# Performance work log

Measured on AMD Instinct MI355X. Metric: run time of the kernel, lower is better.

## Reference

```python
import jax, jax.numpy as jnp
import numpy as np

N = 100000
E = 1600000
F_IN = 512
H1, C1 = 8, 8          # conv1: 8 heads x 8 channels, concat -> 64
H2, C2 = 1, 16         # conv2: 1 head x num_classes=16, mean
NEG_SLOPE = 0.2


def setup_inputs() -> dict:
    key = jax.random.key(0)
    ks = jax.random.split(key, 10)
    x = jax.random.normal(ks[0], (N, F_IN), dtype=jnp.float32)
    edge_index = jax.random.randint(ks[1], (2, E), 0, N, dtype=jnp.int64)
    s1 = 1.0 / np.sqrt(F_IN)
    s2 = 1.0 / np.sqrt(H1 * C1)
    W1 = jax.random.normal(ks[2], (F_IN, H1 * C1), dtype=jnp.float32) * s1
    a1_src = jax.random.normal(ks[3], (H1, C1), dtype=jnp.float32) * 0.1
    a1_dst = jax.random.normal(ks[4], (H1, C1), dtype=jnp.float32) * 0.1
    b1 = jnp.zeros((H1 * C1,), dtype=jnp.float32)
    W2 = jax.random.normal(ks[5], (H1 * C1, H2 * C2), dtype=jnp.float32) * s2
    a2_src = jax.random.normal(ks[6], (H2, C2), dtype=jnp.float32) * 0.1
    a2_dst = jax.random.normal(ks[7], (H2, C2), dtype=jnp.float32) * 0.1
    b2 = jnp.zeros((C2,), dtype=jnp.float32)
    return {"x": x, "edge_index": edge_index, "W1": W1, "a1_src": a1_src,
            "a1_dst": a1_dst, "b1": b1, "W2": W2, "a2_src": a2_src,
            "a2_dst": a2_dst, "b2": b2}


def _add_self_loops(edge_index, n):
    loops = jnp.arange(n, dtype=edge_index.dtype)
    return jnp.concatenate([edge_index, jnp.stack([loops, loops])], axis=1)


def gat_conv(x, edge_index, W, a_src, a_dst, bias, concat):
    # x: [N, Fin]; W: [Fin, H*C]; a_*: [H, C]
    n = x.shape[0]
    H, C = a_src.shape
    h = (x @ W).reshape(n, H, C)                      # [N, H, C]
    al_src = jnp.einsum('nhc,hc->nh', h, a_src)       # [N, H]
    al_dst = jnp.einsum('nhc,hc->nh', h, a_dst)
    src, dst = edge_index[0], edge_index[1]
    e = al_src[src] + al_dst[dst]                     # [E, H]
    e = jnp.where(e > 0, e, NEG_SLOPE * e)            # LeakyReLU
    # segment softmax over destination nodes
    m = jax.ops.segment_max(e, dst, num_segments=n)   # [N, H]
    ex = jnp.exp(e - m[dst])
    s = jax.ops.segment_sum(ex, dst, num_segments=n)  # [N, H]
    alpha = ex / s[dst]                               # [E, H]
    msg = h[src] * alpha[:, :, None]                  # [E, H, C]
    out = jax.ops.segment_sum(msg, dst, num_segments=n)  # [N, H, C]
    if concat:
        out = out.reshape(n, H * C)
    else:
        out = out.mean(axis=1)
    return out + bias


def reference(x, edge_index, W1, a1_src, a1_dst, b1, W2, a2_src, a2_dst, b2):
    ei = _add_self_loops(edge_index, x.shape[0])
    h = gat_conv(x, ei, W1, a1_src, a1_dst, b1, concat=True)
    h = jax.nn.elu(h)
    h = gat_conv(h, ei, W2, a2_src, a2_dst, b2, concat=False)
    return jax.nn.log_softmax(h, axis=1)
```

## Files before the change

### kernel.cpp

```cpp
#include <hip/hip_runtime.h>
#include <math.h>

#define F_IN 512
#define NHEAD1 8
#define NC1 8
#define F1 64
#define NC2 16
#define NEG_SLOPE 0.2f
#define BSHIFT 7
#define PART_G 512
#define BUILD_CAP 4608

static __device__ __forceinline__ float leaky(float v) {
    return v > 0.0f ? v : NEG_SLOPE * v;
}

__global__ __launch_bounds__(256) void k_gemm1(const float* __restrict__ x,
                                               const float* __restrict__ W,
                                               const float* __restrict__ a1s,
                                               const float* __restrict__ a1d,
                                               float* __restrict__ h1,
                                               float* __restrict__ al1s,
                                               float* __restrict__ al1d, int N) {
    __shared__ float xs[32][68];
    __shared__ float wsm[32][64];
    const int tid = threadIdx.x;
    const int tx = tid & 15, ty = tid >> 4;
    const int row0 = blockIdx.x * 64;
    const int r = tid & 63;
    const int kq = tid >> 6;
    float acc[4][4] = {};

    for (int k0 = 0; k0 < F_IN; k0 += 32) {
        {
            int gr = row0 + r;
            float4 v0 = make_float4(0.f, 0.f, 0.f, 0.f), v1 = v0;
            if (gr < N) {
                const float* p = x + (size_t)gr * F_IN + k0 + kq * 8;
                v0 = *(const float4*)p;
                v1 = *(const float4*)(p + 4);
            }
            xs[kq * 8 + 0][r] = v0.x; xs[kq * 8 + 1][r] = v0.y;
            xs[kq * 8 + 2][r] = v0.z; xs[kq * 8 + 3][r] = v0.w;
            xs[kq * 8 + 4][r] = v1.x; xs[kq * 8 + 5][r] = v1.y;
            xs[kq * 8 + 6][r] = v1.z; xs[kq * 8 + 7][r] = v1.w;
            int wr = tid >> 4;
            int wc = (tid & 15) * 4;
            #pragma unroll
            for (int rr = 0; rr < 32; rr += 16) {
                *(float4*)(&wsm[wr + rr][wc]) =
                    *(const float4*)(W + (size_t)(k0 + wr + rr) * F1 + wc);
            }
        }
        __syncthreads();
        #pragma unroll
        for (int k = 0; k < 32; ++k) {
            float4 a = *(const float4*)(&xs[k][ty * 4]);
            float4 b = *(const float4*)(&wsm[k][tx * 4]);
            acc[0][0] = fmaf(a.x, b.x, acc[0][0]); acc[0][1] = fmaf(a.x, b.y, acc[0][1]);
            acc[0][2] = fmaf(a.x, b.z, acc[0][2]); acc[0][3] = fmaf(a.x, b.w, acc[0][3]);
            acc[1][0] = fmaf(a.y, b.x, acc[1][0]); acc[1][1] = fmaf(a.y, b.y, acc[1][1]);
            acc[1][2] = fmaf(a.y, b.z, acc[1][2]); acc[1][3] = fmaf(a.y, b.w, acc[1][3]);
            acc[2][0] = fmaf(a.z, b.x, acc[2][0]); acc[2][1] = fmaf(a.z, b.y, acc[2][1]);
            acc[2][2] = fmaf(a.z, b.z, acc[2][2]); acc[2][3] = fmaf(a.z, b.w, acc[2][3]);
            acc[3][0] = fmaf(a.w, b.x, acc[3][0]); acc[3][1] = fmaf(a.w, b.y, acc[3][1]);
            acc[3][2] = fmaf(a.w, b.z, acc[3][2]); acc[3][3] = fmaf(a.w, b.w, acc[3][3]);
        }
        __syncthreads();
    }
    const int h = tx >> 1;
    const float* as = a1s + h * 8 + (tx & 1) * 4;
    const float* ad = a1d + h * 8 + (tx & 1) * 4;
    float4 asv = *(const float4*)as;
    float4 adv = *(const float4*)ad;
    #pragma unroll
    for (int i = 0; i < 4; ++i) {
        int gr = row0 + ty * 4 + i;
        float ps = acc[i][0] * asv.x + acc[i][1] * asv.y
                 + acc[i][2] * asv.z + acc[i][3] * asv.w;
        float pd = acc[i][0] * adv.x + acc[i][1] * adv.y
                 + acc[i][2] * adv.z + acc[i][3] * adv.w;
        ps += __shfl_xor(ps, 1);
        pd += __shfl_xor(pd, 1);
        if (gr < N) {
            *(float4*)(h1 + (size_t)gr * F1 + tx * 4) =
                make_float4(acc[i][0], acc[i][1], acc[i][2], acc[i][3]);
            if ((tx & 1) == 0) {
                al1s[gr * 8 + h] = ps;
                al1d[gr * 8 + h] = pd;
            }
        }
    }
}

__global__ __launch_bounds__(256) void k_bcount(const int* __restrict__ ei,
                                                int* __restrict__ counts,
                                                int E, int NBUCK, int chunk) {
    __shared__ int cnt[1024];
    const int g = blockIdx.x, tid = threadIdx.x;
    for (int i = tid; i < NBUCK; i += 256) cnt[i] = 0;
    __syncthreads();
    int lo = g * chunk, hi = lo + chunk;
    if (hi > E) hi = E;
    for (int e = lo + tid; e < hi; e += 256)
        atomicAdd(&cnt[ei[E + e] >> BSHIFT], 1);
    __syncthreads();
    for (int k = tid; k < NBUCK; k += 256)
        counts[k * PART_G + g] = cnt[k];
}

__global__ __launch_bounds__(256) void k_scan_block(const int* __restrict__ in,
                                                    int* __restrict__ out,
                                                    int* __restrict__ blocksum, int L) {
    __shared__ int sdata[256];
    int t = threadIdx.x;
    int i = blockIdx.x * 256 + t;
    int v = (i < L) ? in[i] : 0;
    sdata[t] = v;
    __syncthreads();
    for (int off = 1; off < 256; off <<= 1) {
        int add = (t >= off) ? sdata[t - off] : 0;
        __syncthreads();
        sdata[t] += add;
        __syncthreads();
    }
    if (i < L) out[i] = sdata[t] - v;
    if (t == 255) blocksum[blockIdx.x] = sdata[t];
}

__global__ void k_scan_carry(const int* __restrict__ blocksum,
                             int* __restrict__ blockoffset, int NB) {
    int lane = threadIdx.x;
    int carry = 0;
    for (int base = 0; base < NB; base += 64) {
        int i = base + lane;
        int v = (i < NB) ? blocksum[i] : 0;
        int x = v;
        #pragma unroll
        for (int off = 1; off < 64; off <<= 1) {
            int y = __shfl_up(x, off);
            if (lane >= off) x += y;
        }
        if (i < NB) blockoffset[i] = carry + x - v;
        carry += __shfl(x, 63);
    }
}

__global__ __launch_bounds__(256) void k_bscatter(const int* __restrict__ ei,
                                                  const int* __restrict__ offs,
                                                  const int* __restrict__ boff,
                                                  unsigned* __restrict__ packed,
                                                  int E, int NBUCK, int chunk) {
    __shared__ int cur[1024];
    const int g = blockIdx.x, tid = threadIdx.x;
    for (int k = tid; k < NBUCK; k += 256) {
        int idx = k * PART_G + g;
        cur[k] = offs[idx] + boff[idx >> 8];
    }
    __syncthreads();
    int lo = g * chunk, hi = lo + chunk;
    if (hi > E) hi = E;
    for (int e = lo + tid; e < hi; e += 256) {
        int src = ei[e], dst = ei[E + e];
        int pos = atomicAdd(&cur[dst >> BSHIFT], 1);
        packed[pos] = ((unsigned)(dst & 127) << 20) | (unsigned)src;
    }
}

__global__ __launch_bounds__(256) void k_bbuild(const unsigned* __restrict__ packed,
                                                const int* __restrict__ offs,
                                                const int* __restrict__ boff,
                                                int* __restrict__ rowptr,
                                                int* __restrict__ esrc,
                                                int E, int N, int NBUCK) {
    __shared__ int sdeg[128], sinc[128], scur[128];
    __shared__ int sbuf[BUILD_CAP];
    const int k = blockIdx.x, tid = threadIdx.x;
    const int i0 = k * PART_G;
    const int s = offs[i0] + boff[i0 >> 8];
    int e;
    if (k + 1 < NBUCK) {
        int i1 = (k + 1) * PART_G;
        e = offs[i1] + boff[i1 >> 8];
    } else e = E;
    const int cnt = e - s;
    if (tid < 128) sdeg[tid] = 0;
    __syncthreads();
    for (int i = tid; i < cnt; i += 256)
        atomicAdd(&sdeg[packed[s + i] >> 20], 1);
    __syncthreads();
    if (tid < 128) sinc[tid] = sdeg[tid];
    __syncthreads();
    for (int off = 1; off < 128; off <<= 1) {
        int add = (tid < 128 && tid >= off) ? sinc[tid - off] : 0;
        __syncthreads();
        if (tid < 128) sinc[tid] += add;
        __syncthreads();
    }
    int nd = N - (k << BSHIFT);
    if (nd > 128) nd = 128;
    if (tid < nd) {
        int excl = sinc[tid] - sdeg[tid];
        rowptr[(k << BSHIFT) + tid] = s + excl;
        scur[tid] = excl;
    }
    if (k == 0 && tid == 0) rowptr[N] = E;
    __syncthreads();
    if (cnt <= BUILD_CAP) {
        for (int i = tid; i < cnt; i += 256) {
            unsigned p = packed[s + i];
            int pos = atomicAdd(&scur[p >> 20], 1);
            sbuf[pos] = (int)(p & 0xFFFFFu);
        }
        __syncthreads();
        for (int i = tid; i < cnt; i += 256) esrc[s + i] = sbuf[i];
    } else {
        for (int i = tid; i < cnt; i += 256) {
            unsigned p = packed[s + i];
            int pos = atomicAdd(&scur[p >> 20], 1);
            esrc[s + pos] = (int)(p & 0xFFFFFu);
        }
    }
}

__global__ __launch_bounds__(256) void k_agg1(
    const float* __restrict__ h1, const float* __restrict__ al1s,
    const float* __restrict__ al1d, const int* __restrict__ rowptr,
    const int* __restrict__ esrc, const float* __restrict__ b1,
    const float* __restrict__ W2, const float* __restrict__ a2s,
    const float* __restrict__ a2d, float* __restrict__ h2,
    float* __restrict__ al2s, float* __restrict__ al2d, int N) {
    const int lane = threadIdx.x & 63;
    const int wv = threadIdx.x >> 6;
    const int n = blockIdx.x * 4 + wv;
    if (n >= N) return;
    const int sub = lane >> 4;
    const int t = lane & 15;
    const int h = t >> 1;

    float4 w2r[4];
    #pragma unroll
    for (int j = 0; j < 4; ++j)
        w2r[j] = *(const float4*)(W2 + (4 * t + j) * NC2 + 4 * sub);
    const float4 b1v  = *(const float4*)(b1 + 4 * t);
    const float4 a2sv = *(const float4*)(a2s + 4 * sub);
    const float4 a2dv = *(const float4*)(a2d + 4 * sub);

    const float aldh = al1d[n * 8 + h];
    float s = 0.f, acc0 = 0.f, acc1 = 0.f, acc2 = 0.f, acc3 = 0.f;
    if (sub == 0) {
        float w0 = __expf(leaky(al1s[n * 8 + h] + aldh));
        float4 u = *(const float4*)(h1 + (size_t)n * F1 + t * 4);
        s = w0;
        acc0 = w0 * u.x; acc1 = w0 * u.y; acc2 = w0 * u.z; acc3 = w0 * u.w;
    }
    const int start = rowptr[n], end = rowptr[n + 1];
    for (int base = start; base < end; base += 64) {
        int cnt = end - base;
        if (cnt > 64) cnt = 64;
        int msrc = (lane < cnt) ? esrc[base + lane] : 0;
        for (int j4 = 0; j4 < cnt; j4 += 4) {
            int idx = j4 + sub;
            int src = __shfl(msrc, idx);
            float w = (idx < cnt) ? __expf(leaky(al1s[src * 8 + h] + aldh)) : 0.f;
            float4 u = *(const float4*)(h1 + (size_t)src * F1 + t * 4);
            s += w;
            acc0 = fmaf(w, u.x, acc0);
            acc1 = fmaf(w, u.y, acc1);
            acc2 = fmaf(w, u.z, acc2);
            acc3 = fmaf(w, u.w, acc3);
        }
    }
    #pragma unroll
    for (int off = 16; off < 64; off <<= 1) {
        s    += __shfl_xor(s, off);
        acc0 += __shfl_xor(acc0, off);
        acc1 += __shfl_xor(acc1, off);
        acc2 += __shfl_xor(acc2, off);
        acc3 += __shfl_xor(acc3, off);
    }
    float rs = 1.0f / s;
    float v0 = acc0 * rs + b1v.x; v0 = v0 > 0.f ? v0 : expm1f(v0);
    float v1 = acc1 * rs + b1v.y; v1 = v1 > 0.f ? v1 : expm1f(v1);
    float v2 = acc2 * rs + b1v.z; v2 = v2 > 0.f ? v2 : expm1f(v2);
    float v3 = acc3 * rs + b1v.w; v3 = v3 > 0.f ? v3 : expm1f(v3);
    float p0 = v0 * w2r[0].x + v1 * w2r[1].x + v2 * w2r[2].x + v3 * w2r[3].x;
    float p1 = v0 * w2r[0].y + v1 * w2r[1].y + v2 * w2r[2].y + v3 * w2r[3].y;
    float p2 = v0 * w2r[0].z + v1 * w2r[1].z + v2 * w2r[2].z + v3 * w2r[3].z;
    float p3 = v0 * w2r[0].w + v1 * w2r[1].w + v2 * w2r[2].w + v3 * w2r[3].w;
    #pragma unroll
    for (int off = 1; off < 16; off <<= 1) {
        p0 += __shfl_xor(p0, off);
        p1 += __shfl_xor(p1, off);
        p2 += __shfl_xor(p2, off);
        p3 += __shfl_xor(p3, off);
    }
    float ts = p0 * a2sv.x + p1 * a2sv.y + p2 * a2sv.z + p3 * a2sv.w;
    float td = p0 * a2dv.x + p1 * a2dv.y + p2 * a2dv.z + p3 * a2dv.w;
    ts += __shfl_xor(ts, 16); ts += __shfl_xor(ts, 32);
    td += __shfl_xor(td, 16); td += __shfl_xor(td, 32);
    if (t == 0)
        *(float4*)(h2 + (size_t)n * NC2 + sub * 4) = make_float4(p0, p1, p2, p3);
    if (lane == 0) { al2s[n] = ts; al2d[n] = td; }
}

__global__ __launch_bounds__(256) void k_agg2(
    const float* __restrict__ h2, const float* __restrict__ al2s,
    const float* __restrict__ al2d, const int* __restrict__ rowptr,
    const int* __restrict__ esrc, const float* __restrict__ b2,
    float* __restrict__ out, int N) {
    const int lane = threadIdx.x & 63;
    const int wv = threadIdx.x >> 6;
    const int n = blockIdx.x * 4 + wv;
    if (n >= N) return;
    const int sub = lane >> 3;
    const int t = lane & 7;
    const float ald = al2d[n];
    float s = 0.f, a0 = 0.f, a1 = 0.f;
    if (sub == 0) {
        float w0 = __expf(leaky(al2s[n] + ald));
        float2 u = *(const float2*)(h2 + (size_t)n * NC2 + t * 2);
        s = w0;
        a0 = w0 * u.x;
        a1 = w0 * u.y;
    }
    const int start = rowptr[n], end = rowptr[n + 1];
    for (int base = start; base < end; base += 64) {
        int cnt = end - base;
        if (cnt > 64) cnt = 64;
        int msrc = (lane < cnt) ? esrc[base + lane] : 0;
        for (int j8 = 0; j8 < cnt; j8 += 8) {
            int idx = j8 + sub;
            int src = __shfl(msrc, idx);
            float w = (idx < cnt) ? __expf(leaky(al2s[src] + ald)) : 0.f;
            float2 u = *(const float2*)(h2 + (size_t)src * NC2 + t * 2);
            s += w;
            a0 = fmaf(w, u.x, a0);
            a1 = fmaf(w, u.y, a1);
        }
    }
    #pragma unroll
    for (int off = 8; off < 64; off <<= 1) {
        s  += __shfl_xor(s, off);
        a0 += __shfl_xor(a0, off);
        a1 += __shfl_xor(a1, off);
    }
    float rs = 1.0f / s;
    float2 b2v = *(const float2*)(b2 + 2 * t);
    float v0 = a0 * rs + b2v.x;
    float v1 = a1 * rs + b2v.y;
    float mm = fmaxf(v0, v1);
    #pragma unroll
    for (int off = 1; off < 8; off <<= 1) mm = fmaxf(mm, __shfl_xor(mm, off));
    float se = __expf(v0 - mm) + __expf(v1 - mm);
    #pragma unroll
    for (int off = 1; off < 8; off <<= 1) se += __shfl_xor(se, off);
    float l = logf(se) + mm;
    if (sub == 0)
        *(float2*)(out + (size_t)n * NC2 + 2 * t) = make_float2(v0 - l, v1 - l);
}

extern "C" void kernel_launch(void* const* d_in, const int* in_sizes, int n_in,
                              void* d_out, int out_size, void* d_ws, size_t ws_size,
                              hipStream_t stream) {
    const float* x      = (const float*)d_in[0];
    const int*   ei     = (const int*)d_in[1];
    const float* W1     = (const float*)d_in[2];
    const float* a1_src = (const float*)d_in[3];
    const float* a1_dst = (const float*)d_in[4];
    const float* b1     = (const float*)d_in[5];
    const float* W2     = (const float*)d_in[6];
    const float* a2_src = (const float*)d_in[7];
    const float* a2_dst = (const float*)d_in[8];
    const float* b2     = (const float*)d_in[9];
    float* out = (float*)d_out;

    const int N = in_sizes[0] / F_IN;
    const int E = in_sizes[1] / 2;
    const int NH = N * NHEAD1;
    const int NBUCK = (N + 127) >> BSHIFT;
    const int L = NBUCK * PART_G;
    const int NB = (L + 255) / 256;
    const int chunk = (E + PART_G - 1) / PART_G;

    char* base = (char*)d_ws;
    size_t off = 0;
    auto alloc = [&](size_t bytes, size_t align) -> void* {
        off = (off + align - 1) & ~(align - 1);
        void* p = base + off; off += bytes; return p;
    };
    float* h1   = (float*)alloc((size_t)N * F1 * 4, 16);
    float* al1s = (float*)alloc((size_t)NH * 4, 16);
    float* al1d = (float*)alloc((size_t)NH * 4, 16);
    float* h2   = (float*)alloc((size_t)N * NC2 * 4, 16);
    float* al2s = (float*)alloc((size_t)N * 4, 16);
    float* al2d = (float*)alloc((size_t)N * 4, 16);
    int* rowptr = (int*)alloc((size_t)(N + 1) * 4, 16);
    int* esrc   = (int*)alloc((size_t)E * 4, 16);
    char* tbase = (char*)h1;
    unsigned* packed = (unsigned*)tbase;
    int* counts   = (int*)(tbase + (size_t)E * 4);
    int* offs     = counts + L;
    int* blocksum = offs + L;
    int* boffset  = blocksum + NB;

    const int B = 256;
    auto blocks = [](long long cnt, int b) { return (int)((cnt + b - 1) / b); };

    k_bcount<<<PART_G, 256, 0, stream>>>(ei, counts, E, NBUCK, chunk);
    k_scan_block<<<NB, 256, 0, stream>>>(counts, offs, blocksum, L);
    k_scan_carry<<<1, 64, 0, stream>>>(blocksum, boffset, NB);
    k_bscatter<<<PART_G, 256, 0, stream>>>(ei, offs, boffset, packed, E, NBUCK, chunk);
    k_bbuild<<<NBUCK, 256, 0, stream>>>(packed, offs, boffset, rowptr, esrc, E, N, NBUCK);

    k_gemm1<<<dim3((N + 63) / 64), dim3(256), 0, stream>>>(x, W1, a1_src, a1_dst,
                                                           h1, al1s, al1d, N);
    k_agg1<<<blocks(N, 4), 256, 0, stream>>>(h1, al1s, al1d, rowptr, esrc,
                                             b1, W2, a2_src, a2_dst,
                                             h2, al2s, al2d, N);
    k_agg2<<<blocks(N, 4), 256, 0, stream>>>(h2, al2s, al2d, rowptr, esrc, b2, out, N);
}
```

Baseline: 573.2 us.

## Store node features h1 and h2 in fp16 and remap aggregation lanes

The GEMM now writes the layer-1 node features as half precision, and layer 1 writes its transformed features the same way. Both aggregation kernels gather fp16 rows and accumulate in fp32. Lanes are remapped so each lane handles 8 (layer 1) or 4 (layer 2) channels, which lets more edges be processed per wave step. This halves the random-gather traffic and roughly doubles edge parallelism per wave. The cost is fp16 rounding error in the intermediate features and more registers per lane.

```diff
diff --git a/kernel.cpp b/kernel.cpp
--- a/kernel.cpp
+++ b/kernel.cpp
@@ -1,4 +1,5 @@
 #include <hip/hip_runtime.h>
+#include <hip/hip_fp16.h>
 #include <math.h>
 
 #define F_IN 512
@@ -19,7 +20,7 @@
                                                const float* __restrict__ W,
                                                const float* __restrict__ a1s,
                                                const float* __restrict__ a1d,
-                                               float* __restrict__ h1,
+                                               __half* __restrict__ h1h,
                                                float* __restrict__ al1s,
                                                float* __restrict__ al1d, int N) {
     __shared__ float xs[32][68];
@@ -83,8 +84,10 @@
         ps += __shfl_xor(ps, 1);
         pd += __shfl_xor(pd, 1);
         if (gr < N) {
-            *(float4*)(h1 + (size_t)gr * F1 + tx * 4) =
-                make_float4(acc[i][0], acc[i][1], acc[i][2], acc[i][3]);
+            union { __half2 h2v[2]; float2 f; } cv;
+            cv.h2v[0] = __floats2half2_rn(acc[i][0], acc[i][1]);
+            cv.h2v[1] = __floats2half2_rn(acc[i][2], acc[i][3]);
+            *(float2*)(h1h + (size_t)gr * F1 + tx * 4) = cv.f;
             if ((tx & 1) == 0) {
                 al1s[gr * 8 + h] = ps;
                 al1d[gr * 8 + h] = pd;
@@ -224,105 +227,33 @@
 }
 
 __global__ __launch_bounds__(256) void k_agg1(
-    const float* __restrict__ h1, const float* __restrict__ al1s,
+    const __half* __restrict__ h1h, const float* __restrict__ al1s,
     const float* __restrict__ al1d, const int* __restrict__ rowptr,
     const int* __restrict__ esrc, const float* __restrict__ b1,
     const float* __restrict__ W2, const float* __restrict__ a2s,
-    const float* __restrict__ a2d, float* __restrict__ h2,
+    const float* __restrict__ a2d, __half* __restrict__ h2h,
     float* __restrict__ al2s, float* __restrict__ al2d, int N) {
-    const int lane = threadIdx.x & 63;
-    const int wv = threadIdx.x >> 6;
-    const int n = blockIdx.x * 4 + wv;
-    if (n >= N) return;
-    const int sub = lane >> 4;
-    const int t = lane & 15;
-    const int h = t >> 1;
-
-    float4 w2r[4];
-    #pragma unroll
-    for (int j = 0; j < 4; ++j)
-        w2r[j] = *(const float4*)(W2 + (4 * t + j) * NC2 + 4 * sub);
-    const float4 b1v  = *(const float4*)(b1 + 4 * t);
-    const float4 a2sv = *(const float4*)(a2s + 4 * sub);
-    const float4 a2dv = *(const float4*)(a2d + 4 * sub);
-
-    const float aldh = al1d[n * 8 + h];
-    float s = 0.f, acc0 = 0.f, acc1 = 0.f, acc2 = 0.f, acc3 = 0.f;
-    if (sub == 0) {
-        float w0 = __expf(leaky(al1s[n * 8 + h] + aldh));
-        float4 u = *(const float4*)(h1 + (size_t)n * F1 + t * 4);
-        s = w0;
-        acc0 = w0 * u.x; acc1 = w0 * u.y; acc2 = w0 * u.z; acc3 = w0 * u.w;
-    }
-    const int start = rowptr[n], end = rowptr[n + 1];
-    for (int base = start; base < end; base += 64) {
-        int cnt = end - base;
-        if (cnt > 64) cnt = 64;
-        int msrc = (lane < cnt) ? esrc[base + lane] : 0;
-        for (int j4 = 0; j4 < cnt; j4 += 4) {
-            int idx = j4 + sub;
-            int src = __shfl(msrc, idx);
-            float w = (idx < cnt) ? __expf(leaky(al1s[src * 8 + h] + aldh)) : 0.f;
-            float4 u = *(const float4*)(h1 + (size_t)src * F1 + t * 4);
-            s += w;
-            acc0 = fmaf(w, u.x, acc0);
-            acc1 = fmaf(w, u.y, acc1);
-            acc2 = fmaf(w, u.z, acc2);
-            acc3 = fmaf(w, u.w, acc3);
-        }
-    }
-    #pragma unroll
-    for (int off = 16; off < 64; off <<= 1) {
-        s    += __shfl_xor(s, off);
-        acc0 += __shfl_xor(acc0, off);
-        acc1 += __shfl_xor(acc1, off);
-        acc2 += __shfl_xor(acc2, off);
-        acc3 += __shfl_xor(acc3, off);
-    }
-    float rs = 1.0f / s;
-    float v0 = acc0 * rs + b1v.x; v0 = v0 > 0.f ? v0 : expm1f(v0);
-    float v1 = acc1 * rs + b1v.y; v1 = v1 > 0.f ? v1 : expm1f(v1);
-    float v2 = acc2 * rs + b1v.z; v2 = v2 > 0.f ? v2 : expm1f(v2);
-    float v3 = acc3 * rs + b1v.w; v3 = v3 > 0.f ? v3 : expm1f(v3);
-    float p0 = v0 * w2r[0].x + v1 * w2r[1].x + v2 * w2r[2].x + v3 * w2r[3].x;
-    float p1 = v0 * w2r[0].y + v1 * w2r[1].y + v2 * w2r[2].y + v3 * w2r[3].y;
-    float p2 = v0 * w2r[0].z + v1 * w2r[1].z + v2 * w2r[2].z + v3 * w2r[3].z;
-    float p3 = v0 * w2r[0].w + v1 * w2r[1].w + v2 * w2r[2].w + v3 * w2r[3].w;
-    #pragma unroll
-    for (int off = 1; off < 16; off <<= 1) {
-        p0 += __shfl_xor(p0, off);
-        p1 += __shfl_xor(p1, off);
-        p2 += __shfl_xor(p2, off);
-        p3 += __shfl_xor(p3, off);
-    }
-    float ts = p0 * a2sv.x + p1 * a2sv.y + p2 * a2sv.z + p3 * a2sv.w;
-    float td = p0 * a2dv.x + p1 * a2dv.y + p2 * a2dv.z + p3 * a2dv.w;
-    ts += __shfl_xor(ts, 16); ts += __shfl_xor(ts, 32);
-    td += __shfl_xor(td, 16); td += __shfl_xor(td, 32);
-    if (t == 0)
-        *(float4*)(h2 + (size_t)n * NC2 + sub * 4) = make_float4(p0, p1, p2, p3);
-    if (lane == 0) { al2s[n] = ts; al2d[n] = td; }
-}
-
-__global__ __launch_bounds__(256) void k_agg2(
-    const float* __restrict__ h2, const float* __restrict__ al2s,
-    const float* __restrict__ al2d, const int* __restrict__ rowptr,
-    const int* __restrict__ esrc, const float* __restrict__ b2,
-    float* __restrict__ out, int N) {
     const int lane = threadIdx.x & 63;
     const int wv = threadIdx.x >> 6;
     const int n = blockIdx.x * 4 + wv;
     if (n >= N) return;
     const int sub = lane >> 3;
     const int t = lane & 7;
-    const float ald = al2d[n];
-    float s = 0.f, a0 = 0.f, a1 = 0.f;
+
+    const float aldh = al1d[n * 8 + t];
+    float s = 0.f;
+    float acc[8] = {};
     if (sub == 0) {
-        float w0 = __expf(leaky(al2s[n] + ald));
-        float2 u = *(const float2*)(h2 + (size_t)n * NC2 + t * 2);
+        float w0 = __expf(leaky(al1s[n * 8 + t] + aldh));
+        float4 raw = *(const float4*)(h1h + (size_t)n * F1 + t * 8);
+        const __half2* hp = (const __half2*)&raw;
         s = w0;
-        a0 = w0 * u.x;
-        a1 = w0 * u.y;
+        #pragma unroll
+        for (int q = 0; q < 4; ++q) {
+            float2 c = __half22float2(hp[q]);
+            acc[2 * q]     = w0 * c.x;
+            acc[2 * q + 1] = w0 * c.y;
+        }
     }
     const int start = rowptr[n], end = rowptr[n + 1];
     for (int base = start; base < end; base += 64) {
@@ -332,32 +263,127 @@
         for (int j8 = 0; j8 < cnt; j8 += 8) {
             int idx = j8 + sub;
             int src = __shfl(msrc, idx);
+            float w = (idx < cnt) ? __expf(leaky(al1s[src * 8 + t] + aldh)) : 0.f;
+            float4 raw = *(const float4*)(h1h + (size_t)src * F1 + t * 8);
+            const __half2* hp = (const __half2*)&raw;
+            s += w;
+            #pragma unroll
+            for (int q = 0; q < 4; ++q) {
+                float2 c = __half22float2(hp[q]);
+                acc[2 * q]     = fmaf(w, c.x, acc[2 * q]);
+                acc[2 * q + 1] = fmaf(w, c.y, acc[2 * q + 1]);
+            }
+        }
+    }
+    #pragma unroll
+    for (int off = 8; off < 64; off <<= 1) {
+        s += __shfl_xor(s, off);
+        #pragma unroll
+        for (int q = 0; q < 8; ++q) acc[q] += __shfl_xor(acc[q], off);
+    }
+    float rs = 1.0f / s;
+    const float4 b1a = *(const float4*)(b1 + 8 * t);
+    const float4 b1b = *(const float4*)(b1 + 8 * t + 4);
+    float v[8];
+    v[0] = acc[0] * rs + b1a.x; v[1] = acc[1] * rs + b1a.y;
+    v[2] = acc[2] * rs + b1a.z; v[3] = acc[3] * rs + b1a.w;
+    v[4] = acc[4] * rs + b1b.x; v[5] = acc[5] * rs + b1b.y;
+    v[6] = acc[6] * rs + b1b.z; v[7] = acc[7] * rs + b1b.w;
+    #pragma unroll
+    for (int q = 0; q < 8; ++q) v[q] = v[q] > 0.f ? v[q] : expm1f(v[q]);
+    float p0 = 0.f, p1 = 0.f;
+    #pragma unroll
+    for (int c = 0; c < 8; ++c) {
+        float2 wrow = *(const float2*)(W2 + (size_t)(8 * t + c) * NC2 + 2 * sub);
+        p0 = fmaf(v[c], wrow.x, p0);
+        p1 = fmaf(v[c], wrow.y, p1);
+    }
+    #pragma unroll
+    for (int off = 1; off < 8; off <<= 1) {
+        p0 += __shfl_xor(p0, off);
+        p1 += __shfl_xor(p1, off);
+    }
+    const float2 a2sv = *(const float2*)(a2s + 2 * sub);
+    const float2 a2dv = *(const float2*)(a2d + 2 * sub);
+    float ts = p0 * a2sv.x + p1 * a2sv.y;
+    float td = p0 * a2dv.x + p1 * a2dv.y;
+    #pragma unroll
+    for (int off = 8; off < 64; off <<= 1) {
+        ts += __shfl_xor(ts, off);
+        td += __shfl_xor(td, off);
+    }
+    if (t == 0)
+        *(__half2*)(h2h + (size_t)n * NC2 + 2 * sub) = __floats2half2_rn(p0, p1);
+    if (lane == 0) { al2s[n] = ts; al2d[n] = td; }
+}
+
+__global__ __launch_bounds__(256) void k_agg2(
+    const __half* __restrict__ h2h, const float* __restrict__ al2s,
+    const float* __restrict__ al2d, const int* __restrict__ rowptr,
+    const int* __restrict__ esrc, const float* __restrict__ b2,
+    float* __restrict__ out, int N) {
+    const int lane = threadIdx.x & 63;
+    const int wv = threadIdx.x >> 6;
+    const int n = blockIdx.x * 4 + wv;
+    if (n >= N) return;
+    const int sub = lane >> 2;
+    const int t = lane & 3;
+    const float ald = al2d[n];
+    float s = 0.f, a0 = 0.f, a1 = 0.f, a2 = 0.f, a3 = 0.f;
+    if (sub == 0) {
+        float w0 = __expf(leaky(al2s[n] + ald));
+        float2 raw = *(const float2*)(h2h + (size_t)n * NC2 + 4 * t);
+        const __half2* hp = (const __half2*)&raw;
+        float2 c01 = __half22float2(hp[0]);
+        float2 c23 = __half22float2(hp[1]);
+        s = w0;
+        a0 = w0 * c01.x; a1 = w0 * c01.y;
+        a2 = w0 * c23.x; a3 = w0 * c23.y;
+    }
+    const int start = rowptr[n], end = rowptr[n + 1];
+    for (int base = start; base < end; base += 64) {
+        int cnt = end - base;
+        if (cnt > 64) cnt = 64;
+        int msrc = (lane < cnt) ? esrc[base + lane] : 0;
+        for (int j16 = 0; j16 < cnt; j16 += 16) {
+            int idx = j16 + sub;
+            int src = __shfl(msrc, idx);
             float w = (idx < cnt) ? __expf(leaky(al2s[src] + ald)) : 0.f;
-            float2 u = *(const float2*)(h2 + (size_t)src * NC2 + t * 2);
+            float2 raw = *(const float2*)(h2h + (size_t)src * NC2 + 4 * t);
+            const __half2* hp = (const __half2*)&raw;
+            float2 c01 = __half22float2(hp[0]);
+            float2 c23 = __half22float2(hp[1]);
             s += w;
-            a0 = fmaf(w, u.x, a0);
-            a1 = fmaf(w, u.y, a1);
-        }
-    }
-    #pragma unroll
-    for (int off = 8; off < 64; off <<= 1) {
+            a0 = fmaf(w, c01.x, a0);
+            a1 = fmaf(w, c01.y, a1);
+            a2 = fmaf(w, c23.x, a2);
+            a3 = fmaf(w, c23.y, a3);
+        }
+    }
+    #pragma unroll
+    for (int off = 4; off < 64; off <<= 1) {
         s  += __shfl_xor(s, off);
         a0 += __shfl_xor(a0, off);
         a1 += __shfl_xor(a1, off);
+        a2 += __shfl_xor(a2, off);
+        a3 += __shfl_xor(a3, off);
     }
     float rs = 1.0f / s;
-    float2 b2v = *(const float2*)(b2 + 2 * t);
+    const float4 b2v = *(const float4*)(b2 + 4 * t);
     float v0 = a0 * rs + b2v.x;
     float v1 = a1 * rs + b2v.y;
-    float mm = fmaxf(v0, v1);
-    #pragma unroll
-    for (int off = 1; off < 8; off <<= 1) mm = fmaxf(mm, __shfl_xor(mm, off));
-    float se = __expf(v0 - mm) + __expf(v1 - mm);
-    #pragma unroll
-    for (int off = 1; off < 8; off <<= 1) se += __shfl_xor(se, off);
+    float v2 = a2 * rs + b2v.z;
+    float v3 = a3 * rs + b2v.w;
+    float mm = fmaxf(fmaxf(v0, v1), fmaxf(v2, v3));
+    #pragma unroll
+    for (int off = 1; off < 4; off <<= 1) mm = fmaxf(mm, __shfl_xor(mm, off));
+    float se = __expf(v0 - mm) + __expf(v1 - mm) + __expf(v2 - mm) + __expf(v3 - mm);
+    #pragma unroll
+    for (int off = 1; off < 4; off <<= 1) se += __shfl_xor(se, off);
     float l = logf(se) + mm;
     if (sub == 0)
-        *(float2*)(out + (size_t)n * NC2 + 2 * t) = make_float2(v0 - l, v1 - l);
+        *(float4*)(out + (size_t)n * NC2 + 4 * t) =
+            make_float4(v0 - l, v1 - l, v2 - l, v3 - l);
 }
 
 extern "C" void kernel_launch(void* const* d_in, const int* in_sizes, int n_in,
@@ -389,22 +415,21 @@
         off = (off + align - 1) & ~(align - 1);
         void* p = base + off; off += bytes; return p;
     };
-    float* h1   = (float*)alloc((size_t)N * F1 * 4, 16);
+    __half* h1h = (__half*)alloc((size_t)N * F1 * 2, 16);
     float* al1s = (float*)alloc((size_t)NH * 4, 16);
     float* al1d = (float*)alloc((size_t)NH * 4, 16);
-    float* h2   = (float*)alloc((size_t)N * NC2 * 4, 16);
+    __half* h2h = (__half*)alloc((size_t)N * NC2 * 2, 16);
     float* al2s = (float*)alloc((size_t)N * 4, 16);
     float* al2d = (float*)alloc((size_t)N * 4, 16);
     int* rowptr = (int*)alloc((size_t)(N + 1) * 4, 16);
     int* esrc   = (int*)alloc((size_t)E * 4, 16);
-    char* tbase = (char*)h1;
+    char* tbase = (char*)h1h;
     unsigned* packed = (unsigned*)tbase;
     int* counts   = (int*)(tbase + (size_t)E * 4);
     int* offs     = counts + L;
     int* blocksum = offs + L;
     int* boffset  = blocksum + NB;
 
-    const int B = 256;
     auto blocks = [](long long cnt, int b) { return (int)((cnt + b - 1) / b); };
 
     k_bcount<<<PART_G, 256, 0, stream>>>(ei, counts, E, NBUCK, chunk);
@@ -414,9 +439,9 @@
     k_bbuild<<<NBUCK, 256, 0, stream>>>(packed, offs, boffset, rowptr, esrc, E, N, NBUCK);
 
     k_gemm1<<<dim3((N + 63) / 64), dim3(256), 0, stream>>>(x, W1, a1_src, a1_dst,
-                                                           h1, al1s, al1d, N);
-    k_agg1<<<blocks(N, 4), 256, 0, stream>>>(h1, al1s, al1d, rowptr, esrc,
+                                                           h1h, al1s, al1d, N);
+    k_agg1<<<blocks(N, 4), 256, 0, stream>>>(h1h, al1s, al1d, rowptr, esrc,
                                              b1, W2, a2_src, a2_dst,
-                                             h2, al2s, al2d, N);
-    k_agg2<<<blocks(N, 4), 256, 0, stream>>>(h2, al2s, al2d, rowptr, esrc, b2, out, N);
-}
+                                             h2h, al2s, al2d, N);
+    k_agg2<<<blocks(N, 4), 256, 0, stream>>>(h2h, al2s, al2d, rowptr, esrc, b2, out, N);
+}
```

New measurement: 584.3 us. About the same (+1.9%).

## Use fp16 MFMA for first-layer GEMM and store layer-2 features in half

Applied to the files above, without the earlier changes.

Rewrites the x@W1 GEMM to convert inputs to fp16 and use the 16x16x32 f16 MFMA instruction, with a small prep kernel that transposes W1 to fp16. The second-layer features h2 are stored as half, and k_agg2 gives each lane 4 channels so 16 edges are processed per pass instead of 8. The intent is to replace slow scalar FP32 FMA with matrix cores and halve gather bandwidth in agg2, at the cost of fp16 rounding error.

```diff
diff --git a/kernel.cpp b/kernel.cpp
--- a/kernel.cpp
+++ b/kernel.cpp
@@ -1,4 +1,5 @@
 #include <hip/hip_runtime.h>
+#include <hip/hip_fp16.h>
 #include <math.h>
 
 #define F_IN 512
@@ -11,83 +12,97 @@
 #define PART_G 512
 #define BUILD_CAP 4608
 
+typedef _Float16 v8h __attribute__((ext_vector_type(8)));
+typedef float v4f __attribute__((ext_vector_type(4)));
+
 static __device__ __forceinline__ float leaky(float v) {
     return v > 0.0f ? v : NEG_SLOPE * v;
 }
 
+__global__ __launch_bounds__(256) void k_prep(const float* __restrict__ W,
+                                              _Float16* __restrict__ w1t) {
+    int idx = blockIdx.x * 256 + threadIdx.x;
+    if (idx < 64 * 512) {
+        int c = idx >> 9, k = idx & 511;
+        w1t[idx] = (_Float16)W[k * 64 + c];
+    }
+}
+
 __global__ __launch_bounds__(256) void k_gemm1(const float* __restrict__ x,
-                                               const float* __restrict__ W,
+                                               const _Float16* __restrict__ w1t,
                                                const float* __restrict__ a1s,
                                                const float* __restrict__ a1d,
                                                float* __restrict__ h1,
                                                float* __restrict__ al1s,
                                                float* __restrict__ al1d, int N) {
-    __shared__ float xs[32][68];
-    __shared__ float wsm[32][64];
+    __shared__ _Float16 xs[64][72];
+    __shared__ _Float16 ws[64][72];
     const int tid = threadIdx.x;
-    const int tx = tid & 15, ty = tid >> 4;
+    const int lane = tid & 63;
+    const int wv = tid >> 6;
     const int row0 = blockIdx.x * 64;
-    const int r = tid & 63;
-    const int kq = tid >> 6;
-    float acc[4][4] = {};
-
-    for (int k0 = 0; k0 < F_IN; k0 += 32) {
-        {
-            int gr = row0 + r;
-            float4 v0 = make_float4(0.f, 0.f, 0.f, 0.f), v1 = v0;
+    const int srow = tid >> 2;
+    const int skq = (tid & 3) * 16;
+    v4f acc[4] = {};
+
+    for (int k0 = 0; k0 < F_IN; k0 += 64) {
+        int gr = row0 + srow;
+        float4 v0, v1, v2, v3;
+        if (gr < N) {
+            const float* p = x + (size_t)gr * F_IN + k0 + skq;
+            v0 = *(const float4*)p;       v1 = *(const float4*)(p + 4);
+            v2 = *(const float4*)(p + 8); v3 = *(const float4*)(p + 12);
+        } else {
+            v0 = make_float4(0.f, 0.f, 0.f, 0.f); v1 = v0; v2 = v0; v3 = v0;
+        }
+        const _Float16* q = w1t + (size_t)srow * F_IN + k0 + skq;
+        v8h wa = *(const v8h*)q;
+        v8h wb = *(const v8h*)(q + 8);
+        v8h xa, xb;
+        xa[0] = (_Float16)v0.x; xa[1] = (_Float16)v0.y;
+        xa[2] = (_Float16)v0.z; xa[3] = (_Float16)v0.w;
+        xa[4] = (_Float16)v1.x; xa[5] = (_Float16)v1.y;
+        xa[6] = (_Float16)v1.z; xa[7] = (_Float16)v1.w;
+        xb[0] = (_Float16)v2.x; xb[1] = (_Float16)v2.y;
+        xb[2] = (_Float16)v2.z; xb[3] = (_Float16)v2.w;
+        xb[4] = (_Float16)v3.x; xb[5] = (_Float16)v3.y;
+        xb[6] = (_Float16)v3.z; xb[7] = (_Float16)v3.w;
+        __syncthreads();
+        *(v8h*)&xs[srow][skq]     = xa;
+        *(v8h*)&xs[srow][skq + 8] = xb;
+        *(v8h*)&ws[srow][skq]     = wa;
+        *(v8h*)&ws[srow][skq + 8] = wb;
+        __syncthreads();
+        #pragma unroll
+        for (int kk = 0; kk < 64; kk += 32) {
+            v8h a = *(const v8h*)&xs[wv * 16 + (lane & 15)][kk + (lane >> 4) * 8];
+            #pragma unroll
+            for (int c4 = 0; c4 < 4; ++c4) {
+                v8h b = *(const v8h*)&ws[c4 * 16 + (lane & 15)][kk + (lane >> 4) * 8];
+                acc[c4] = __builtin_amdgcn_mfma_f32_16x16x32_f16(a, b, acc[c4], 0, 0, 0);
+            }
+        }
+    }
+    const int g = lane >> 4;
+    const int cl = lane & 15;
+    #pragma unroll
+    for (int c4 = 0; c4 < 4; ++c4) {
+        float asv = a1s[c4 * 16 + cl];
+        float adv = a1d[c4 * 16 + cl];
+        #pragma unroll
+        for (int r = 0; r < 4; ++r) {
+            int gr = row0 + wv * 16 + g * 4 + r;
+            float vacc = acc[c4][r];
+            float ps = vacc * asv, pd = vacc * adv;
+            ps += __shfl_xor(ps, 1); ps += __shfl_xor(ps, 2); ps += __shfl_xor(ps, 4);
+            pd += __shfl_xor(pd, 1); pd += __shfl_xor(pd, 2); pd += __shfl_xor(pd, 4);
             if (gr < N) {
-                const float* p = x + (size_t)gr * F_IN + k0 + kq * 8;
-                v0 = *(const float4*)p;
-                v1 = *(const float4*)(p + 4);
-            }
-            xs[kq * 8 + 0][r] = v0.x; xs[kq * 8 + 1][r] = v0.y;
-            xs[kq * 8 + 2][r] = v0.z; xs[kq * 8 + 3][r] = v0.w;
-            xs[kq * 8 + 4][r] = v1.x; xs[kq * 8 + 5][r] = v1.y;
-            xs[kq * 8 + 6][r] = v1.z; xs[kq * 8 + 7][r] = v1.w;
-            int wr = tid >> 4;
-            int wc = (tid & 15) * 4;
-            #pragma unroll
-            for (int rr = 0; rr < 32; rr += 16) {
-                *(float4*)(&wsm[wr + rr][wc]) =
-                    *(const float4*)(W + (size_t)(k0 + wr + rr) * F1 + wc);
-            }
-        }
-        __syncthreads();
-        #pragma unroll
-        for (int k = 0; k < 32; ++k) {
-            float4 a = *(const float4*)(&xs[k][ty * 4]);
-            float4 b = *(const float4*)(&wsm[k][tx * 4]);
-            acc[0][0] = fmaf(a.x, b.x, acc[0][0]); acc[0][1] = fmaf(a.x, b.y, acc[0][1]);
-            acc[0][2] = fmaf(a.x, b.z, acc[0][2]); acc[0][3] = fmaf(a.x, b.w, acc[0][3]);
-            acc[1][0] = fmaf(a.y, b.x, acc[1][0]); acc[1][1] = fmaf(a.y, b.y, acc[1][1]);
-            acc[1][2] = fmaf(a.y, b.z, acc[1][2]); acc[1][3] = fmaf(a.y, b.w, acc[1][3]);
-            acc[2][0] = fmaf(a.z, b.x, acc[2][0]); acc[2][1] = fmaf(a.z, b.y, acc[2][1]);
-            acc[2][2] = fmaf(a.z, b.z, acc[2][2]); acc[2][3] = fmaf(a.z, b.w, acc[2][3]);
-            acc[3][0] = fmaf(a.w, b.x, acc[3][0]); acc[3][1] = fmaf(a.w, b.y, acc[3][1]);
-            acc[3][2] = fmaf(a.w, b.z, acc[3][2]); acc[3][3] = fmaf(a.w, b.w, acc[3][3]);
-        }
-        __syncthreads();
-    }
-    const int h = tx >> 1;
-    const float* as = a1s + h * 8 + (tx & 1) * 4;
-    const float* ad = a1d + h * 8 + (tx & 1) * 4;
-    float4 asv = *(const float4*)as;
-    float4 adv = *(const float4*)ad;
-    #pragma unroll
-    for (int i = 0; i < 4; ++i) {
-        int gr = row0 + ty * 4 + i;
-        float ps = acc[i][0] * asv.x + acc[i][1] * asv.y
-                 + acc[i][2] * asv.z + acc[i][3] * asv.w;
-        float pd = acc[i][0] * adv.x + acc[i][1] * adv.y
-                 + acc[i][2] * adv.z + acc[i][3] * adv.w;
-        ps += __shfl_xor(ps, 1);
-        pd += __shfl_xor(pd, 1);
-        if (gr < N) {
-            *(float4*)(h1 + (size_t)gr * F1 + tx * 4) =
-                make_float4(acc[i][0], acc[i][1], acc[i][2], acc[i][3]);
-            if ((tx & 1) == 0) {
-                al1s[gr * 8 + h] = ps;
-                al1d[gr * 8 + h] = pd;
+                h1[(size_t)gr * F1 + c4 * 16 + cl] = vacc;
+                if ((lane & 7) == 0) {
+                    int head = c4 * 2 + (cl >> 3);
+                    al1s[gr * 8 + head] = ps;
+                    al1d[gr * 8 + head] = pd;
+                }
             }
         }
     }
@@ -228,7 +243,7 @@
     const float* __restrict__ al1d, const int* __restrict__ rowptr,
     const int* __restrict__ esrc, const float* __restrict__ b1,
     const float* __restrict__ W2, const float* __restrict__ a2s,
-    const float* __restrict__ a2d, float* __restrict__ h2,
+    const float* __restrict__ a2d, __half* __restrict__ h2h,
     float* __restrict__ al2s, float* __restrict__ al2d, int N) {
     const int lane = threadIdx.x & 63;
     const int wv = threadIdx.x >> 6;
@@ -299,13 +314,17 @@
     float td = p0 * a2dv.x + p1 * a2dv.y + p2 * a2dv.z + p3 * a2dv.w;
     ts += __shfl_xor(ts, 16); ts += __shfl_xor(ts, 32);
     td += __shfl_xor(td, 16); td += __shfl_xor(td, 32);
-    if (t == 0)
-        *(float4*)(h2 + (size_t)n * NC2 + sub * 4) = make_float4(p0, p1, p2, p3);
+    if (t == 0) {
+        union { __half2 h2v[2]; float2 f; } cv;
+        cv.h2v[0] = __floats2half2_rn(p0, p1);
+        cv.h2v[1] = __floats2half2_rn(p2, p3);
+        *(float2*)(h2h + (size_t)n * NC2 + sub * 4) = cv.f;
+    }
     if (lane == 0) { al2s[n] = ts; al2d[n] = td; }
 }
 
 __global__ __launch_bounds__(256) void k_agg2(
-    const float* __restrict__ h2, const float* __restrict__ al2s,
+    const __half* __restrict__ h2h, const float* __restrict__ al2s,
     const float* __restrict__ al2d, const int* __restrict__ rowptr,
     const int* __restrict__ esrc, const float* __restrict__ b2,
     float* __restrict__ out, int N) {
@@ -313,51 +332,64 @@
     const int wv = threadIdx.x >> 6;
     const int n = blockIdx.x * 4 + wv;
     if (n >= N) return;
-    const int sub = lane >> 3;
-    const int t = lane & 7;
+    const int sub = lane >> 2;
+    const int t = lane & 3;
     const float ald = al2d[n];
-    float s = 0.f, a0 = 0.f, a1 = 0.f;
+    float s = 0.f, a0 = 0.f, a1 = 0.f, a2 = 0.f, a3 = 0.f;
     if (sub == 0) {
         float w0 = __expf(leaky(al2s[n] + ald));
-        float2 u = *(const float2*)(h2 + (size_t)n * NC2 + t * 2);
+        float2 raw0 = *(const float2*)(h2h + (size_t)n * NC2 + 4 * t);
+        const __half2* hp = (const __half2*)&raw0;
+        float2 c01 = __half22float2(hp[0]);
+        float2 c23 = __half22float2(hp[1]);
         s = w0;
-        a0 = w0 * u.x;
-        a1 = w0 * u.y;
+        a0 = w0 * c01.x; a1 = w0 * c01.y;
+        a2 = w0 * c23.x; a3 = w0 * c23.y;
     }
     const int start = rowptr[n], end = rowptr[n + 1];
     for (int base = start; base < end; base += 64) {
         int cnt = end - base;
         if (cnt > 64) cnt = 64;
         int msrc = (lane < cnt) ? esrc[base + lane] : 0;
-        for (int j8 = 0; j8 < cnt; j8 += 8) {
-            int idx = j8 + sub;
+        for (int j16 = 0; j16 < cnt; j16 += 16) {
+            int idx = j16 + sub;
             int src = __shfl(msrc, idx);
             float w = (idx < cnt) ? __expf(leaky(al2s[src] + ald)) : 0.f;
-            float2 u = *(const float2*)(h2 + (size_t)src * NC2 + t * 2);
+            float2 raw = *(const float2*)(h2h + (size_t)src * NC2 + 4 * t);
+            const __half2* hp = (const __half2*)&raw;
+            float2 c01 = __half22float2(hp[0]);
+            float2 c23 = __half22float2(hp[1]);
             s += w;
-            a0 = fmaf(w, u.x, a0);
-            a1 = fmaf(w, u.y, a1);
-        }
-    }
-    #pragma unroll
-    for (int off = 8; off < 64; off <<= 1) {
+            a0 = fmaf(w, c01.x, a0);
+            a1 = fmaf(w, c01.y, a1);
+            a2 = fmaf(w, c23.x, a2);
+            a3 = fmaf(w, c23.y, a3);
+        }
+    }
+    #pragma unroll
+    for (int off = 4; off < 64; off <<= 1) {
         s  += __shfl_xor(s, off);
         a0 += __shfl_xor(a0, off);
         a1 += __shfl_xor(a1, off);
+        a2 += __shfl_xor(a2, off);
+        a3 += __shfl_xor(a3, off);
     }
     float rs = 1.0f / s;
-    float2 b2v = *(const float2*)(b2 + 2 * t);
+    const float4 b2v = *(const float4*)(b2 + 4 * t);
     float v0 = a0 * rs + b2v.x;
     float v1 = a1 * rs + b2v.y;
-    float mm = fmaxf(v0, v1);
-    #pragma unroll
-    for (int off = 1; off < 8; off <<= 1) mm = fmaxf(mm, __shfl_xor(mm, off));
-    float se = __expf(v0 - mm) + __expf(v1 - mm);
-    #pragma unroll
-    for (int off = 1; off < 8; off <<= 1) se += __shfl_xor(se, off);
+    float v2 = a2 * rs + b2v.z;
+    float v3 = a3 * rs + b2v.w;
+    float mm = fmaxf(fmaxf(v0, v1), fmaxf(v2, v3));
+    #pragma unroll
+    for (int off = 1; off < 4; off <<= 1) mm = fmaxf(mm, __shfl_xor(mm, off));
+    float se = __expf(v0 - mm) + __expf(v1 - mm) + __expf(v2 - mm) + __expf(v3 - mm);
+    #pragma unroll
+    for (int off = 1; off < 4; off <<= 1) se += __shfl_xor(se, off);
     float l = logf(se) + mm;
     if (sub == 0)
-        *(float2*)(out + (size_t)n * NC2 + 2 * t) = make_float2(v0 - l, v1 - l);
+        *(float4*)(out + (size_t)n * NC2 + 4 * t) =
+            make_float4(v0 - l, v1 - l, v2 - l, v3 - l);
 }
 
 extern "C" void kernel_launch(void* const* d_in, const int* in_sizes, int n_in,
@@ -392,11 +424,12 @@
     float* h1   = (float*)alloc((size_t)N * F1 * 4, 16);
     float* al1s = (float*)alloc((size_t)NH * 4, 16);
     float* al1d = (float*)alloc((size_t)NH * 4, 16);
-    float* h2   = (float*)alloc((size_t)N * NC2 * 4, 16);
+    __half* h2h = (__half*)alloc((size_t)N * NC2 * 2, 16);
     float* al2s = (float*)alloc((size_t)N * 4, 16);
     float* al2d = (float*)alloc((size_t)N * 4, 16);
     int* rowptr = (int*)alloc((size_t)(N + 1) * 4, 16);
     int* esrc   = (int*)alloc((size_t)E * 4, 16);
+    _Float16* w1t = (_Float16*)alloc((size_t)64 * F_IN * 2, 16);
     char* tbase = (char*)h1;
     unsigned* packed = (unsigned*)tbase;
     int* counts   = (int*)(tbase + (size_t)E * 4);
@@ -404,7 +437,6 @@
     int* blocksum = offs + L;
     int* boffset  = blocksum + NB;
 
-    const int B = 256;
     auto blocks = [](long long cnt, int b) { return (int)((cnt + b - 1) / b); };
 
     k_bcount<<<PART_G, 256, 0, stream>>>(ei, counts, E, NBUCK, chunk);
@@ -413,10 +445,11 @@
     k_bscatter<<<PART_G, 256, 0, stream>>>(ei, offs, boffset, packed, E, NBUCK, chunk);
     k_bbuild<<<NBUCK, 256, 0, stream>>>(packed, offs, boffset, rowptr, esrc, E, N, NBUCK);
 
-    k_gemm1<<<dim3((N + 63) / 64), dim3(256), 0, stream>>>(x, W1, a1_src, a1_dst,
+    k_prep<<<128, 256, 0, stream>>>(W1, w1t);
+    k_gemm1<<<dim3((N + 63) / 64), dim3(256), 0, stream>>>(x, w1t, a1_src, a1_dst,
                                                            h1, al1s, al1d, N);
     k_agg1<<<blocks(N, 4), 256, 0, stream>>>(h1, al1s, al1d, rowptr, esrc,
                                              b1, W2, a2_src, a2_dst,
-                                             h2, al2s, al2d, N);
-    k_agg2<<<blocks(N, 4), 256, 0, stream>>>(h2, al2s, al2d, rowptr, esrc, b2, out, N);
-}
+                                             h2h, al2s, al2d, N);
+    k_agg2<<<blocks(N, 4), 256, 0, stream>>>(h2h, al2s, al2d, rowptr, esrc, b2, out, N);
+}
```

Result: faster. 544.7 us (-5.0%).
